# Optimization experiments

Measured on AMD Instinct MI355X. Metric: run time of the kernel, lower is better.

Reference implementation:

```python
import jax, jax.numpy as jnp
import numpy as np

B, T, C, H = 32, 500, 256, 8  # batch, seq, n_embd(=in_c), heads


def setup_inputs() -> dict:
    key = jax.random.key(0)
    ks = jax.random.split(key, 6)
    s = 0.02
    return {
        "x": jax.random.normal(ks[0], (B, T, C), dtype=jnp.float32),
        # nn.Linear(in_c, 3*n_embd): store as [in, out] for x @ W
        "W_attn": jax.random.normal(ks[1], (C, 3 * C), dtype=jnp.float32) * s,
        "b_attn": jnp.zeros((3 * C,), dtype=jnp.float32),
        # nn.Conv1d(heads, 1, 1, bias=False): a per-head mixing weight [H]
        "p_w": jax.random.normal(ks[2], (H,), dtype=jnp.float32) * s,
        # nn.Linear(n_embd, n_embd)
        "W_proj": jax.random.normal(ks[3], (C, C), dtype=jnp.float32) * s,
        "b_proj": jnp.zeros((C,), dtype=jnp.float32),
    }


def reference(x, W_attn, b_attn, p_w, W_proj, b_proj):
    Bx, Tx, Cx = x.shape
    Hh = p_w.shape[0]
    d = Cx // Hh
    qkv = x @ W_attn + b_attn                          # [B,T,3C]
    q, k, v = jnp.split(qkv, 3, axis=-1)
    # [B,T,C] -> [B,H,T,d]
    q = q.reshape(Bx, Tx, Hh, d).transpose(0, 2, 1, 3)
    k = k.reshape(Bx, Tx, Hh, d).transpose(0, 2, 1, 3)
    v = v.reshape(Bx, Tx, Hh, d).transpose(0, 2, 1, 3)
    scale = 1.0 / np.sqrt(d).astype(np.float32)
    att = jnp.einsum('bhtd,bhsd->bhts', q, k) * scale  # [B,H,T,T]
    # bias buffer is all ones for T<=500, so masked_fill is a no-op
    # pred path: 1x1 conv over heads (weighted sum), then sigmoid
    pred_weight = jax.nn.sigmoid(jnp.einsum('bhts,h->bts', att, p_w))  # [B,T,T]
    pred_weight = jnp.where(jnp.isnan(pred_weight), 0.0, pred_weight)
    # value path: softmax @ V
    a = jax.nn.softmax(att, axis=-1)                   # [B,H,T,T]
    ctx = jnp.einsum('bhts,bhsd->bhtd', a, v)          # [B,H,T,d]
    ctx = ctx.transpose(0, 2, 1, 3).reshape(Bx, Tx, Cx)  # [B,T,C]
    value = ctx @ W_proj + b_proj
    return (pred_weight, value)
```

## Files before the change

kernel.cpp:

```cpp
#include <hip/hip_runtime.h>
#include <stddef.h>

typedef unsigned short u16;
typedef unsigned int u32;
typedef __attribute__((ext_vector_type(4))) float f32x4;
typedef __attribute__((ext_vector_type(8))) u16 u16x8;
typedef __attribute__((ext_vector_type(8))) short s16x8;
typedef __attribute__((ext_vector_type(2))) u32 u32x2;
typedef __attribute__((ext_vector_type(4))) u32 u32x4;

#define MFMA16 __builtin_amdgcn_mfma_f32_16x16x32_bf16

__device__ __forceinline__ float bf2f(u16 u) { return __uint_as_float(((u32)u) << 16); }
__device__ __forceinline__ u16 f2bf(float f) {
  u32 u = __float_as_uint(f);
  return (u16)((u + 0x7FFFu + ((u >> 16) & 1u)) >> 16);
}
__device__ __forceinline__ u32 cvt_pk_bf16(float lo, float hi) {
  u32 r; asm("v_cvt_pk_bf16_f32 %0, %1, %2" : "=v"(r) : "v"(lo), "v"(hi)); return r;
}
__device__ __forceinline__ float lo16f(u32 v) { return __uint_as_float(v << 16); }
__device__ __forceinline__ float hi16f(u32 v) { return __uint_as_float(v & 0xffff0000u); }

union frag_u { u32x4 u; s16x8 s; };


__global__ __launch_bounds__(256) void convert_x(
    const float* __restrict__ x, u16* __restrict__ xb)
{
  size_t i = ((size_t)blockIdx.x * 256 + threadIdx.x) * 8;
  f32x4 a = *(const f32x4*)&x[i];
  f32x4 b = *(const f32x4*)&x[i + 4];
  u32x4 o;
  o[0] = cvt_pk_bf16(a[0], a[1]); o[1] = cvt_pk_bf16(a[2], a[3]);
  o[2] = cvt_pk_bf16(b[0], b[1]); o[3] = cvt_pk_bf16(b[2], b[3]);
  *(u32x4*)&xb[i] = o;
}

__global__ __launch_bounds__(256) void gemm_qkv(
    const u16* __restrict__ xbA, const float* __restrict__ W,
    const float* __restrict__ bias, u16* __restrict__ qkbuf, u16* __restrict__ vt)
{
  __shared__ u16 As[128][32];
  __shared__ u16 Bs[64][40];
  const int tid = threadIdx.x;
  const int lane = tid & 63;
  const int w = tid >> 6;
  const int cl = lane & 15, g = lane >> 4;
  const int m0 = blockIdx.x * 128, n0 = blockIdx.y * 64;
  const int wm = w >> 1, wn = w & 1;
  const int bn = tid & 63, bk8 = (tid >> 6) * 8;
  const int ar0 = tid >> 2, ac0 = (tid & 3) * 8;
  const int ar1 = (tid + 256) >> 2, ac1 = ((tid + 256) & 3) * 8;

  f32x4 acc[4][2];
#pragma unroll
  for (int mi = 0; mi < 4; ++mi)
#pragma unroll
    for (int ni = 0; ni < 2; ++ni) acc[mi][ni] = (f32x4){0.f, 0.f, 0.f, 0.f};

  for (int kt = 0; kt < 8; ++kt) {
    const int k0 = kt * 32;
    u16x8 a0 = *(const u16x8*)&xbA[(size_t)(m0 + ar0) * 256 + k0 + ac0];
    u16x8 a1 = *(const u16x8*)&xbA[(size_t)(m0 + ar1) * 256 + k0 + ac1];
    float wv[8];
#pragma unroll
    for (int j = 0; j < 8; ++j)
      wv[j] = W[(size_t)(k0 + bk8 + j) * 768 + n0 + bn];
    __syncthreads();
    *(u16x8*)&As[ar0][ac0] = a0;
    *(u16x8*)&As[ar1][ac1] = a1;
    u32x4 bw;
    bw[0] = cvt_pk_bf16(wv[0], wv[1]); bw[1] = cvt_pk_bf16(wv[2], wv[3]);
    bw[2] = cvt_pk_bf16(wv[4], wv[5]); bw[3] = cvt_pk_bf16(wv[6], wv[7]);
    *(u32x4*)&Bs[bn][bk8] = bw;
    __syncthreads();
    s16x8 af[4], bfr[2];
#pragma unroll
    for (int mi = 0; mi < 4; ++mi) af[mi] = *(const s16x8*)&As[wm * 64 + mi * 16 + cl][g * 8];
#pragma unroll
    for (int ni = 0; ni < 2; ++ni) bfr[ni] = *(const s16x8*)&Bs[wn * 32 + ni * 16 + cl][g * 8];
#pragma unroll
    for (int mi = 0; mi < 4; ++mi)
#pragma unroll
      for (int ni = 0; ni < 2; ++ni)
        acc[mi][ni] = MFMA16(af[mi], bfr[ni], acc[mi][ni], 0, 0, 0);
  }
  float bb[2] = { bias[n0 + wn * 32 + cl], bias[n0 + wn * 32 + 16 + cl] };
  if (n0 < 512) {
#pragma unroll
    for (int mi = 0; mi < 4; ++mi)
#pragma unroll
      for (int ni = 0; ni < 2; ++ni)
#pragma unroll
        for (int r = 0; r < 4; ++r) {
          int m = m0 + wm * 64 + mi * 16 + g * 4 + r;
          qkbuf[(size_t)m * 512 + n0 + wn * 32 + ni * 16 + cl] = f2bf(acc[mi][ni][r] + bb[ni]);
        }
  } else {
#pragma unroll
    for (int mi = 0; mi < 4; ++mi)
#pragma unroll
      for (int ni = 0; ni < 2; ++ni) {
        int cb = n0 - 512 + wn * 32 + ni * 16 + cl;
#pragma unroll
        for (int r = 0; r < 4; ++r) {
          int m = m0 + wm * 64 + mi * 16 + g * 4 + r;
          int b2 = m / 500;
          int t2 = m - b2 * 500;
          vt[(size_t)(b2 * 256 + cb) * 500 + t2] = f2bf(acc[mi][ni][r] + bb[ni]);
        }
      }
  }
}

__global__ __launch_bounds__(256) void gemm_proj(
    const u16* __restrict__ A, const float* __restrict__ W,
    const float* __restrict__ bias, float* __restrict__ out)
{
  __shared__ u16 As[128][32];
  __shared__ u16 Bs[64][40];
  const int tid = threadIdx.x;
  const int lane = tid & 63;
  const int w = tid >> 6;
  const int cl = lane & 15, g = lane >> 4;
  const int m0 = blockIdx.x * 128, n0 = blockIdx.y * 64;
  const int wm = w >> 1, wn = w & 1;
  const int bn = tid & 63, bk8 = (tid >> 6) * 8;
  const int ar0 = tid >> 2, ac0 = (tid & 3) * 8;
  const int ar1 = (tid + 256) >> 2, ac1 = ((tid + 256) & 3) * 8;

  f32x4 acc[4][2];
#pragma unroll
  for (int mi = 0; mi < 4; ++mi)
#pragma unroll
    for (int ni = 0; ni < 2; ++ni) acc[mi][ni] = (f32x4){0.f, 0.f, 0.f, 0.f};

  for (int kt = 0; kt < 8; ++kt) {
    const int k0 = kt * 32;
    u16x8 a0 = *(const u16x8*)&A[(size_t)(m0 + ar0) * 256 + k0 + ac0];
    u16x8 a1 = *(const u16x8*)&A[(size_t)(m0 + ar1) * 256 + k0 + ac1];
    float wv[8];
#pragma unroll
    for (int j = 0; j < 8; ++j)
      wv[j] = W[(size_t)(k0 + bk8 + j) * 256 + n0 + bn];
    __syncthreads();
    *(u16x8*)&As[ar0][ac0] = a0;
    *(u16x8*)&As[ar1][ac1] = a1;
    u32x4 bw;
    bw[0] = cvt_pk_bf16(wv[0], wv[1]); bw[1] = cvt_pk_bf16(wv[2], wv[3]);
    bw[2] = cvt_pk_bf16(wv[4], wv[5]); bw[3] = cvt_pk_bf16(wv[6], wv[7]);
    *(u32x4*)&Bs[bn][bk8] = bw;
    __syncthreads();
    s16x8 af[4], bfr[2];
#pragma unroll
    for (int mi = 0; mi < 4; ++mi) af[mi] = *(const s16x8*)&As[wm * 64 + mi * 16 + cl][g * 8];
#pragma unroll
    for (int ni = 0; ni < 2; ++ni) bfr[ni] = *(const s16x8*)&Bs[wn * 32 + ni * 16 + cl][g * 8];
#pragma unroll
    for (int mi = 0; mi < 4; ++mi)
#pragma unroll
      for (int ni = 0; ni < 2; ++ni)
        acc[mi][ni] = MFMA16(af[mi], bfr[ni], acc[mi][ni], 0, 0, 0);
  }
  float bb[2] = { bias[n0 + wn * 32 + cl], bias[n0 + wn * 32 + 16 + cl] };
#pragma unroll
  for (int mi = 0; mi < 4; ++mi)
#pragma unroll
    for (int ni = 0; ni < 2; ++ni)
#pragma unroll
      for (int r = 0; r < 4; ++r) {
        int m = m0 + wm * 64 + mi * 16 + g * 4 + r;
        out[(size_t)m * 256 + n0 + wn * 32 + ni * 16 + cl] = acc[mi][ni][r] + bb[ni];
      }
}

__global__ __launch_bounds__(512, 3) void attn_mfma2(
    const u16* __restrict__ qk, const u16* __restrict__ vt,
    const float* __restrict__ pw_g, float* __restrict__ pred, u16* __restrict__ ctx)
{
  __shared__ u32 pred_lds[8][64][20];
  const int tid = threadIdx.x;
  const int w = tid >> 6;
  const int lane = tid & 63;
  const int cl = lane & 15;
  const int g = lane >> 4;
  const int lin = blockIdx.x;
  const int b = (lin & 7) * 4 + ((lin >> 3) >> 4);
  const int t0 = ((lin >> 3) & 15) * 32;
  const float scale = 0.17677669529663687f;
  const float pwh = pw_g[w] * scale;

  const u16* qkb = qk + (size_t)b * 500 * 512;
  const u16* vtb = vt + (size_t)b * 256 * 500;

  s16x8 qf[2];
#pragma unroll
  for (int qi = 0; qi < 2; ++qi) {
    int tq = t0 + qi * 16 + cl; if (tq > 499) tq = 499;
    qf[qi] = *(const s16x8*)&qkb[(size_t)tq * 512 + w * 32 + g * 8];
  }
  s16x8 onesf;
#pragma unroll
  for (int j = 0; j < 8; ++j) onesf[j] = (short)0x3F80;

  f32x4 of[2][2], lf[2];
#pragma unroll
  for (int qi = 0; qi < 2; ++qi) {
    lf[qi] = (f32x4){0.f, 0.f, 0.f, 0.f};
    of[qi][0] = (f32x4){0.f, 0.f, 0.f, 0.f};
    of[qi][1] = (f32x4){0.f, 0.f, 0.f, 0.f};
  }

  const int rq = tid >> 4;
  const int rs4 = tid & 15;
  const int rsrc = (rs4 & 3) * 16 + (rq & 15);
  const int ridx = (rq >> 4) * 8 + (rs4 >> 2) * 2;
  const int sA = (g & 1) * 32 + cl;
  const int sB = sA + 16;
  const bool hiHalf = (lane >= 32);

#pragma unroll 1
  for (int st = 0; st < 8; ++st) {
    const int s0 = st * 64;
    f32x4 St[2][4];
    {
      s16x8 kf[4];
#pragma unroll
      for (int si = 0; si < 4; ++si) {
        int sr = s0 + si * 16 + cl; if (sr > 499) sr = 499;
        kf[si] = *(const s16x8*)&qkb[(size_t)sr * 512 + 256 + w * 32 + g * 8];
      }
      const f32x4 zf = (f32x4){0.f, 0.f, 0.f, 0.f};
#pragma unroll
      for (int qi = 0; qi < 2; ++qi)
#pragma unroll
        for (int si = 0; si < 4; ++si)
          St[qi][si] = MFMA16(kf[si], qf[qi], zf, 0, 0, 0);
    }
    s16x8 vf[2][2];
#pragma unroll
    for (int di = 0; di < 2; ++di)
#pragma unroll
      for (int s32 = 0; s32 < 2; ++s32) {
        int sv = s0 + s32 * 32 + g * 8; if (sv > 499) sv = 464;
        vf[di][s32] = *(const s16x8*)&vtb[(size_t)(w * 32 + di * 16 + cl) * 500 + sv];
      }
    u32 P2[2][4][2], PD[2][4][2];
#pragma unroll
    for (int qi = 0; qi < 2; ++qi)
#pragma unroll
      for (int si = 0; si < 4; ++si) {
        float pv[4], pdv[4];
#pragma unroll
        for (int r = 0; r < 4; ++r) {
          int sidx = s0 + si * 16 + g * 4 + r;
          float sraw = St[qi][si][r];
          pdv[r] = sraw * pwh;
          float e = __expf(sraw * scale);
          pv[r] = (sidx < 500) ? e : 0.f;
        }
        P2[qi][si][0] = cvt_pk_bf16(pv[0], pv[1]);
        P2[qi][si][1] = cvt_pk_bf16(pv[2], pv[3]);
        PD[qi][si][0] = cvt_pk_bf16(pdv[0], pdv[1]);
        PD[qi][si][1] = cvt_pk_bf16(pdv[2], pdv[3]);
      }
    {
      u32* wp = &pred_lds[w][lane][0];
      u32x4 v0, v1, v2, v3;
      v0[0] = PD[0][0][0]; v0[1] = PD[0][0][1]; v0[2] = PD[0][1][0]; v0[3] = PD[0][1][1];
      v1[0] = PD[0][2][0]; v1[1] = PD[0][2][1]; v1[2] = PD[0][3][0]; v1[3] = PD[0][3][1];
      v2[0] = PD[1][0][0]; v2[1] = PD[1][0][1]; v2[2] = PD[1][1][0]; v2[3] = PD[1][1][1];
      v3[0] = PD[1][2][0]; v3[1] = PD[1][2][1]; v3[2] = PD[1][3][0]; v3[3] = PD[1][3][1];
      *(u32x4*)(wp + 0) = v0;  *(u32x4*)(wp + 4) = v1;
      *(u32x4*)(wp + 8) = v2;  *(u32x4*)(wp + 12) = v3;
    }
#pragma unroll
    for (int s32 = 0; s32 < 2; ++s32) {
#pragma unroll
      for (int qi = 0; qi < 2; ++qi) {
        u32 Z0 = hiHalf ? P2[qi][2 * s32 + 1][0] : P2[qi][2 * s32][0];
        u32 Z1 = hiHalf ? P2[qi][2 * s32 + 1][1] : P2[qi][2 * s32][1];
        frag_u fu;
        fu.u[0] = (u32)__shfl((int)Z0, sA);
        fu.u[1] = (u32)__shfl((int)Z1, sA);
        fu.u[2] = (u32)__shfl((int)Z0, sB);
        fu.u[3] = (u32)__shfl((int)Z1, sB);
        of[qi][0] = MFMA16(fu.s, vf[0][s32], of[qi][0], 0, 0, 0);
        of[qi][1] = MFMA16(fu.s, vf[1][s32], of[qi][1], 0, 0, 0);
        lf[qi] = MFMA16(fu.s, onesf, lf[qi], 0, 0, 0);
      }
    }
    __syncthreads();
    {
      float a0 = 0.f, a1 = 0.f, a2 = 0.f, a3 = 0.f;
#pragma unroll
      for (int w8 = 0; w8 < 8; ++w8) {
        u32x2 v = *(const u32x2*)&pred_lds[w8][rsrc][ridx];
        a0 += lo16f(v[0]); a1 += hi16f(v[0]);
        a2 += lo16f(v[1]); a3 += hi16f(v[1]);
      }
      int tq = t0 + rq, ss = s0 + rs4 * 4;
      if (tq < 500 && ss < 500) {
        f32x4 o;
        o[0] = 1.f / (1.f + __expf(-a0));
        o[1] = 1.f / (1.f + __expf(-a1));
        o[2] = 1.f / (1.f + __expf(-a2));
        o[3] = 1.f / (1.f + __expf(-a3));
        *(f32x4*)&pred[(size_t)(b * 500 + tq) * 500 + ss] = o;
      }
    }
    __syncthreads();
  }
#pragma unroll
  for (int qi = 0; qi < 2; ++qi)
#pragma unroll
    for (int r = 0; r < 4; ++r) {
      int tq = t0 + qi * 16 + g * 4 + r;
      if (tq < 500) {
        float inv = 1.f / lf[qi][r];
        ctx[(size_t)(b * 500 + tq) * 256 + w * 32 + cl]      = f2bf(of[qi][0][r] * inv);
        ctx[(size_t)(b * 500 + tq) * 256 + w * 32 + 16 + cl] = f2bf(of[qi][1][r] * inv);
      }
    }
}

extern "C" void kernel_launch(void* const* d_in, const int* in_sizes, int n_in,
                              void* d_out, int out_size, void* d_ws, size_t ws_size,
                              hipStream_t stream)
{
  const float* x      = (const float*)d_in[0];
  const float* W_attn = (const float*)d_in[1];
  const float* b_attn = (const float*)d_in[2];
  const float* p_w    = (const float*)d_in[3];
  const float* W_proj = (const float*)d_in[4];
  const float* b_proj = (const float*)d_in[5];

  float* pred   = (float*)d_out;
  float* valout = pred + 8000000;

  u16* xb    = (u16*)d_ws;
  u16* ctx   = xb;
  u16* vt    = (u16*)((char*)d_ws + 8192000);
  u16* qkbuf = (u16*)((char*)d_ws + 16384000);

  hipLaunchKernelGGL(convert_x, dim3(2000), dim3(256), 0, stream, x, xb);
  hipLaunchKernelGGL(gemm_qkv, dim3(125, 12), dim3(256), 0, stream,
                     xb, W_attn, b_attn, qkbuf, vt);
  hipLaunchKernelGGL(attn_mfma2, dim3(512), dim3(512), 0, stream,
                     qkbuf, vt, p_w, pred, ctx);
  hipLaunchKernelGGL(gemm_proj, dim3(125, 4), dim3(256), 0, stream,
                     ctx, W_proj, b_proj, valout);
}
```

Measured before the change: 93.68 us.

## Split fused attention into separate pred GEMM and value-attention kernels

Replaces the single fused attention kernel, which reduced per-head scores across waves through LDS with two block barriers per step, with two kernels. The first computes the head-weighted pred scores as a GEMM over all heads, scaling each per-head MFMA partial by p_w. The second handles softmax@V per head with a shuffle-reduced row sum instead of an MFMA against a ones vector. It also folds the fp32-to-bf16 conversion of x into the QKV GEMM load, dropping the convert kernel. The trade-off is recomputing QK^T in both kernels and one extra launch.

```diff
diff --git a/kernel.cpp b/kernel.cpp
--- a/kernel.cpp
+++ b/kernel.cpp
@@ -6,7 +6,6 @@
 typedef __attribute__((ext_vector_type(4))) float f32x4;
 typedef __attribute__((ext_vector_type(8))) u16 u16x8;
 typedef __attribute__((ext_vector_type(8))) short s16x8;
-typedef __attribute__((ext_vector_type(2))) u32 u32x2;
 typedef __attribute__((ext_vector_type(4))) u32 u32x4;
 
 #define MFMA16 __builtin_amdgcn_mfma_f32_16x16x32_bf16
@@ -19,26 +18,12 @@
 __device__ __forceinline__ u32 cvt_pk_bf16(float lo, float hi) {
   u32 r; asm("v_cvt_pk_bf16_f32 %0, %1, %2" : "=v"(r) : "v"(lo), "v"(hi)); return r;
 }
-__device__ __forceinline__ float lo16f(u32 v) { return __uint_as_float(v << 16); }
-__device__ __forceinline__ float hi16f(u32 v) { return __uint_as_float(v & 0xffff0000u); }
 
 union frag_u { u32x4 u; s16x8 s; };
 
 
-__global__ __launch_bounds__(256) void convert_x(
-    const float* __restrict__ x, u16* __restrict__ xb)
-{
-  size_t i = ((size_t)blockIdx.x * 256 + threadIdx.x) * 8;
-  f32x4 a = *(const f32x4*)&x[i];
-  f32x4 b = *(const f32x4*)&x[i + 4];
-  u32x4 o;
-  o[0] = cvt_pk_bf16(a[0], a[1]); o[1] = cvt_pk_bf16(a[2], a[3]);
-  o[2] = cvt_pk_bf16(b[0], b[1]); o[3] = cvt_pk_bf16(b[2], b[3]);
-  *(u32x4*)&xb[i] = o;
-}
-
 __global__ __launch_bounds__(256) void gemm_qkv(
-    const u16* __restrict__ xbA, const float* __restrict__ W,
+    const float* __restrict__ x, const float* __restrict__ W,
     const float* __restrict__ bias, u16* __restrict__ qkbuf, u16* __restrict__ vt)
 {
   __shared__ u16 As[128][32];
@@ -61,15 +46,22 @@
 
   for (int kt = 0; kt < 8; ++kt) {
     const int k0 = kt * 32;
-    u16x8 a0 = *(const u16x8*)&xbA[(size_t)(m0 + ar0) * 256 + k0 + ac0];
-    u16x8 a1 = *(const u16x8*)&xbA[(size_t)(m0 + ar1) * 256 + k0 + ac1];
+    f32x4 a0l = *(const f32x4*)&x[(size_t)(m0 + ar0) * 256 + k0 + ac0];
+    f32x4 a0h = *(const f32x4*)&x[(size_t)(m0 + ar0) * 256 + k0 + ac0 + 4];
+    f32x4 a1l = *(const f32x4*)&x[(size_t)(m0 + ar1) * 256 + k0 + ac1];
+    f32x4 a1h = *(const f32x4*)&x[(size_t)(m0 + ar1) * 256 + k0 + ac1 + 4];
     float wv[8];
 #pragma unroll
     for (int j = 0; j < 8; ++j)
       wv[j] = W[(size_t)(k0 + bk8 + j) * 768 + n0 + bn];
     __syncthreads();
-    *(u16x8*)&As[ar0][ac0] = a0;
-    *(u16x8*)&As[ar1][ac1] = a1;
+    u32x4 p0, p1;
+    p0[0] = cvt_pk_bf16(a0l[0], a0l[1]); p0[1] = cvt_pk_bf16(a0l[2], a0l[3]);
+    p0[2] = cvt_pk_bf16(a0h[0], a0h[1]); p0[3] = cvt_pk_bf16(a0h[2], a0h[3]);
+    p1[0] = cvt_pk_bf16(a1l[0], a1l[1]); p1[1] = cvt_pk_bf16(a1l[2], a1l[3]);
+    p1[2] = cvt_pk_bf16(a1h[0], a1h[1]); p1[3] = cvt_pk_bf16(a1h[2], a1h[3]);
+    *(u32x4*)&As[ar0][ac0] = p0;
+    *(u32x4*)&As[ar1][ac1] = p1;
     u32x4 bw;
     bw[0] = cvt_pk_bf16(wv[0], wv[1]); bw[1] = cvt_pk_bf16(wv[2], wv[3]);
     bw[2] = cvt_pk_bf16(wv[4], wv[5]); bw[3] = cvt_pk_bf16(wv[6], wv[7]);
@@ -111,6 +103,177 @@
           vt[(size_t)(b2 * 256 + cb) * 500 + t2] = f2bf(acc[mi][ni][r] + bb[ni]);
         }
       }
+  }
+}
+
+__global__ __launch_bounds__(256) void pred_gemm(
+    const u16* __restrict__ qk, const float* __restrict__ pw_g,
+    float* __restrict__ pred)
+{
+  const int tid = threadIdx.x;
+  const int lane = tid & 63;
+  const int w = tid >> 6;
+  const int cl = lane & 15, g = lane >> 4;
+  const int lin = blockIdx.x;
+  const int xcd = lin & 7, idx = lin >> 3;
+  const int b = xcd * 4 + (idx >> 4);
+  const int tile = idx & 15;
+  const int tm = tile >> 2, tn = tile & 3;
+  const int r0 = tm * 128 + (w >> 1) * 64;
+  const int c0 = tn * 128 + (w & 1) * 64;
+  const float scale = 0.17677669529663687f;
+
+  const u16* qkb = qk + (size_t)b * 500 * 512;
+  float fw[8];
+#pragma unroll
+  for (int h = 0; h < 8; ++h) fw[h] = pw_g[h] * scale;
+
+  f32x4 acc[4][4];
+#pragma unroll
+  for (int mi = 0; mi < 4; ++mi)
+#pragma unroll
+    for (int ni = 0; ni < 4; ++ni) acc[mi][ni] = (f32x4){0.f, 0.f, 0.f, 0.f};
+
+#pragma unroll 2
+  for (int kt = 0; kt < 8; ++kt) {
+    const int k0 = kt * 32;
+    s16x8 af[4], bf[4];
+#pragma unroll
+    for (int mi = 0; mi < 4; ++mi) {
+      int t = r0 + mi * 16 + cl; if (t > 499) t = 499;
+      af[mi] = *(const s16x8*)&qkb[(size_t)t * 512 + k0 + g * 8];
+    }
+#pragma unroll
+    for (int ni = 0; ni < 4; ++ni) {
+      int s = c0 + ni * 16 + cl; if (s > 499) s = 499;
+      bf[ni] = *(const s16x8*)&qkb[(size_t)s * 512 + 256 + k0 + g * 8];
+    }
+    const f32x4 zf = (f32x4){0.f, 0.f, 0.f, 0.f};
+    const float f = fw[kt];
+#pragma unroll
+    for (int mi = 0; mi < 4; ++mi)
+#pragma unroll
+      for (int ni = 0; ni < 4; ++ni) {
+        f32x4 part = MFMA16(af[mi], bf[ni], zf, 0, 0, 0);
+#pragma unroll
+        for (int r = 0; r < 4; ++r) acc[mi][ni][r] = fmaf(f, part[r], acc[mi][ni][r]);
+      }
+  }
+#pragma unroll
+  for (int mi = 0; mi < 4; ++mi)
+#pragma unroll
+    for (int ni = 0; ni < 4; ++ni) {
+      const int s = c0 + ni * 16 + cl;
+#pragma unroll
+      for (int r = 0; r < 4; ++r) {
+        const int t = r0 + mi * 16 + g * 4 + r;
+        if (t < 500 && s < 500) {
+          pred[(size_t)(b * 500 + t) * 500 + s] =
+              1.f / (1.f + __expf(-acc[mi][ni][r]));
+        }
+      }
+    }
+}
+
+__global__ __launch_bounds__(256) void attn_value(
+    const u16* __restrict__ qk, const u16* __restrict__ vt, u16* __restrict__ ctx)
+{
+  const int tid = threadIdx.x;
+  const int w = tid >> 6;
+  const int lane = tid & 63;
+  const int cl = lane & 15, g = lane >> 4;
+  const int lin = blockIdx.x;
+  const int xcd = lin & 7, idx = lin >> 3;
+  const int b = xcd * 4 + (idx >> 5);
+  const int rem = idx & 31;
+  const int h = rem >> 2, qg = rem & 3;
+  const int t0 = qg * 128 + w * 32;
+  const float scale = 0.17677669529663687f;
+
+  const u16* qkb = qk + (size_t)b * 500 * 512;
+  const u16* vtb = vt + (size_t)b * 256 * 500;
+
+  s16x8 qf[2];
+#pragma unroll
+  for (int qi = 0; qi < 2; ++qi) {
+    int tq = t0 + qi * 16 + cl; if (tq > 499) tq = 499;
+    qf[qi] = *(const s16x8*)&qkb[(size_t)tq * 512 + h * 32 + g * 8];
+  }
+  f32x4 of[2][2];
+  float lsum[2] = {0.f, 0.f};
+#pragma unroll
+  for (int qi = 0; qi < 2; ++qi) {
+    of[qi][0] = (f32x4){0.f, 0.f, 0.f, 0.f};
+    of[qi][1] = (f32x4){0.f, 0.f, 0.f, 0.f};
+  }
+  const int sA = (g & 1) * 32 + cl;
+  const int sB = sA + 16;
+  const bool hiHalf = (lane >= 32);
+
+#pragma unroll 1
+  for (int st = 0; st < 8; ++st) {
+    const int s0 = st * 64;
+    s16x8 kf[4];
+#pragma unroll
+    for (int si = 0; si < 4; ++si) {
+      int sr = s0 + si * 16 + cl; if (sr > 499) sr = 499;
+      kf[si] = *(const s16x8*)&qkb[(size_t)sr * 512 + 256 + h * 32 + g * 8];
+    }
+    s16x8 vf[2][2];
+#pragma unroll
+    for (int di = 0; di < 2; ++di)
+#pragma unroll
+      for (int s32 = 0; s32 < 2; ++s32)
+        vf[di][s32] = *(const s16x8*)&vtb[(size_t)(h * 32 + di * 16 + cl) * 500 +
+                                          s0 + s32 * 32 + g * 8];
+    const f32x4 zf = (f32x4){0.f, 0.f, 0.f, 0.f};
+    u32 P2[2][4][2];
+#pragma unroll
+    for (int qi = 0; qi < 2; ++qi) {
+#pragma unroll
+      for (int si = 0; si < 4; ++si) {
+        f32x4 St = MFMA16(kf[si], qf[qi], zf, 0, 0, 0);
+        float pv[4];
+#pragma unroll
+        for (int r = 0; r < 4; ++r) {
+          int sidx = s0 + si * 16 + g * 4 + r;
+          float e = __expf(St[r] * scale);
+          pv[r] = (sidx < 500) ? e : 0.f;
+          lsum[qi] += pv[r];
+        }
+        P2[qi][si][0] = cvt_pk_bf16(pv[0], pv[1]);
+        P2[qi][si][1] = cvt_pk_bf16(pv[2], pv[3]);
+      }
+    }
+#pragma unroll
+    for (int s32 = 0; s32 < 2; ++s32) {
+#pragma unroll
+      for (int qi = 0; qi < 2; ++qi) {
+        u32 Z0 = hiHalf ? P2[qi][2 * s32 + 1][0] : P2[qi][2 * s32][0];
+        u32 Z1 = hiHalf ? P2[qi][2 * s32 + 1][1] : P2[qi][2 * s32][1];
+        frag_u fu;
+        fu.u[0] = (u32)__shfl((int)Z0, sA);
+        fu.u[1] = (u32)__shfl((int)Z1, sA);
+        fu.u[2] = (u32)__shfl((int)Z0, sB);
+        fu.u[3] = (u32)__shfl((int)Z1, sB);
+        of[qi][0] = MFMA16(fu.s, vf[0][s32], of[qi][0], 0, 0, 0);
+        of[qi][1] = MFMA16(fu.s, vf[1][s32], of[qi][1], 0, 0, 0);
+      }
+    }
+  }
+#pragma unroll
+  for (int qi = 0; qi < 2; ++qi) {
+    float l2 = lsum[qi] + __shfl_xor(lsum[qi], 16);
+    l2 += __shfl_xor(l2, 32);
+#pragma unroll
+    for (int r = 0; r < 4; ++r) {
+      const int tq = t0 + qi * 16 + g * 4 + r;
+      if (tq < 500) {
+        const float inv = 1.f / __shfl(l2, g * 4 + r);
+        ctx[(size_t)(b * 500 + tq) * 256 + h * 32 + cl]      = f2bf(of[qi][0][r] * inv);
+        ctx[(size_t)(b * 500 + tq) * 256 + h * 32 + 16 + cl] = f2bf(of[qi][1][r] * inv);
+      }
+    }
   }
 }
 
@@ -175,156 +338,6 @@
       }
 }
 
-__global__ __launch_bounds__(512, 3) void attn_mfma2(
-    const u16* __restrict__ qk, const u16* __restrict__ vt,
-    const float* __restrict__ pw_g, float* __restrict__ pred, u16* __restrict__ ctx)
-{
-  __shared__ u32 pred_lds[8][64][20];
-  const int tid = threadIdx.x;
-  const int w = tid >> 6;
-  const int lane = tid & 63;
-  const int cl = lane & 15;
-  const int g = lane >> 4;
-  const int lin = blockIdx.x;
-  const int b = (lin & 7) * 4 + ((lin >> 3) >> 4);
-  const int t0 = ((lin >> 3) & 15) * 32;
-  const float scale = 0.17677669529663687f;
-  const float pwh = pw_g[w] * scale;
-
-  const u16* qkb = qk + (size_t)b * 500 * 512;
-  const u16* vtb = vt + (size_t)b * 256 * 500;
-
-  s16x8 qf[2];
-#pragma unroll
-  for (int qi = 0; qi < 2; ++qi) {
-    int tq = t0 + qi * 16 + cl; if (tq > 499) tq = 499;
-    qf[qi] = *(const s16x8*)&qkb[(size_t)tq * 512 + w * 32 + g * 8];
-  }
-  s16x8 onesf;
-#pragma unroll
-  for (int j = 0; j < 8; ++j) onesf[j] = (short)0x3F80;
-
-  f32x4 of[2][2], lf[2];
-#pragma unroll
-  for (int qi = 0; qi < 2; ++qi) {
-    lf[qi] = (f32x4){0.f, 0.f, 0.f, 0.f};
-    of[qi][0] = (f32x4){0.f, 0.f, 0.f, 0.f};
-    of[qi][1] = (f32x4){0.f, 0.f, 0.f, 0.f};
-  }
-
-  const int rq = tid >> 4;
-  const int rs4 = tid & 15;
-  const int rsrc = (rs4 & 3) * 16 + (rq & 15);
-  const int ridx = (rq >> 4) * 8 + (rs4 >> 2) * 2;
-  const int sA = (g & 1) * 32 + cl;
-  const int sB = sA + 16;
-  const bool hiHalf = (lane >= 32);
-
-#pragma unroll 1
-  for (int st = 0; st < 8; ++st) {
-    const int s0 = st * 64;
-    f32x4 St[2][4];
-    {
-      s16x8 kf[4];
-#pragma unroll
-      for (int si = 0; si < 4; ++si) {
-        int sr = s0 + si * 16 + cl; if (sr > 499) sr = 499;
-        kf[si] = *(const s16x8*)&qkb[(size_t)sr * 512 + 256 + w * 32 + g * 8];
-      }
-      const f32x4 zf = (f32x4){0.f, 0.f, 0.f, 0.f};
-#pragma unroll
-      for (int qi = 0; qi < 2; ++qi)
-#pragma unroll
-        for (int si = 0; si < 4; ++si)
-          St[qi][si] = MFMA16(kf[si], qf[qi], zf, 0, 0, 0);
-    }
-    s16x8 vf[2][2];
-#pragma unroll
-    for (int di = 0; di < 2; ++di)
-#pragma unroll
-      for (int s32 = 0; s32 < 2; ++s32) {
-        int sv = s0 + s32 * 32 + g * 8; if (sv > 499) sv = 464;
-        vf[di][s32] = *(const s16x8*)&vtb[(size_t)(w * 32 + di * 16 + cl) * 500 + sv];
-      }
-    u32 P2[2][4][2], PD[2][4][2];
-#pragma unroll
-    for (int qi = 0; qi < 2; ++qi)
-#pragma unroll
-      for (int si = 0; si < 4; ++si) {
-        float pv[4], pdv[4];
-#pragma unroll
-        for (int r = 0; r < 4; ++r) {
-          int sidx = s0 + si * 16 + g * 4 + r;
-          float sraw = St[qi][si][r];
-          pdv[r] = sraw * pwh;
-          float e = __expf(sraw * scale);
-          pv[r] = (sidx < 500) ? e : 0.f;
-        }
-        P2[qi][si][0] = cvt_pk_bf16(pv[0], pv[1]);
-        P2[qi][si][1] = cvt_pk_bf16(pv[2], pv[3]);
-        PD[qi][si][0] = cvt_pk_bf16(pdv[0], pdv[1]);
-        PD[qi][si][1] = cvt_pk_bf16(pdv[2], pdv[3]);
-      }
-    {
-      u32* wp = &pred_lds[w][lane][0];
-      u32x4 v0, v1, v2, v3;
-      v0[0] = PD[0][0][0]; v0[1] = PD[0][0][1]; v0[2] = PD[0][1][0]; v0[3] = PD[0][1][1];
-      v1[0] = PD[0][2][0]; v1[1] = PD[0][2][1]; v1[2] = PD[0][3][0]; v1[3] = PD[0][3][1];
-      v2[0] = PD[1][0][0]; v2[1] = PD[1][0][1]; v2[2] = PD[1][1][0]; v2[3] = PD[1][1][1];
-      v3[0] = PD[1][2][0]; v3[1] = PD[1][2][1]; v3[2] = PD[1][3][0]; v3[3] = PD[1][3][1];
-      *(u32x4*)(wp + 0) = v0;  *(u32x4*)(wp + 4) = v1;
-      *(u32x4*)(wp + 8) = v2;  *(u32x4*)(wp + 12) = v3;
-    }
-#pragma unroll
-    for (int s32 = 0; s32 < 2; ++s32) {
-#pragma unroll
-      for (int qi = 0; qi < 2; ++qi) {
-        u32 Z0 = hiHalf ? P2[qi][2 * s32 + 1][0] : P2[qi][2 * s32][0];
-        u32 Z1 = hiHalf ? P2[qi][2 * s32 + 1][1] : P2[qi][2 * s32][1];
-        frag_u fu;
-        fu.u[0] = (u32)__shfl((int)Z0, sA);
-        fu.u[1] = (u32)__shfl((int)Z1, sA);
-        fu.u[2] = (u32)__shfl((int)Z0, sB);
-        fu.u[3] = (u32)__shfl((int)Z1, sB);
-        of[qi][0] = MFMA16(fu.s, vf[0][s32], of[qi][0], 0, 0, 0);
-        of[qi][1] = MFMA16(fu.s, vf[1][s32], of[qi][1], 0, 0, 0);
-        lf[qi] = MFMA16(fu.s, onesf, lf[qi], 0, 0, 0);
-      }
-    }
-    __syncthreads();
-    {
-      float a0 = 0.f, a1 = 0.f, a2 = 0.f, a3 = 0.f;
-#pragma unroll
-      for (int w8 = 0; w8 < 8; ++w8) {
-        u32x2 v = *(const u32x2*)&pred_lds[w8][rsrc][ridx];
-        a0 += lo16f(v[0]); a1 += hi16f(v[0]);
-        a2 += lo16f(v[1]); a3 += hi16f(v[1]);
-      }
-      int tq = t0 + rq, ss = s0 + rs4 * 4;
-      if (tq < 500 && ss < 500) {
-        f32x4 o;
-        o[0] = 1.f / (1.f + __expf(-a0));
-        o[1] = 1.f / (1.f + __expf(-a1));
-        o[2] = 1.f / (1.f + __expf(-a2));
-        o[3] = 1.f / (1.f + __expf(-a3));
-        *(f32x4*)&pred[(size_t)(b * 500 + tq) * 500 + ss] = o;
-      }
-    }
-    __syncthreads();
-  }
-#pragma unroll
-  for (int qi = 0; qi < 2; ++qi)
-#pragma unroll
-    for (int r = 0; r < 4; ++r) {
-      int tq = t0 + qi * 16 + g * 4 + r;
-      if (tq < 500) {
-        float inv = 1.f / lf[qi][r];
-        ctx[(size_t)(b * 500 + tq) * 256 + w * 32 + cl]      = f2bf(of[qi][0][r] * inv);
-        ctx[(size_t)(b * 500 + tq) * 256 + w * 32 + 16 + cl] = f2bf(of[qi][1][r] * inv);
-      }
-    }
-}
-
 extern "C" void kernel_launch(void* const* d_in, const int* in_sizes, int n_in,
                               void* d_out, int out_size, void* d_ws, size_t ws_size,
                               hipStream_t stream)
@@ -339,16 +352,16 @@
   float* pred   = (float*)d_out;
   float* valout = pred + 8000000;
 
-  u16* xb    = (u16*)d_ws;
-  u16* ctx   = xb;
-  u16* vt    = (u16*)((char*)d_ws + 8192000);
-  u16* qkbuf = (u16*)((char*)d_ws + 16384000);
-
-  hipLaunchKernelGGL(convert_x, dim3(2000), dim3(256), 0, stream, x, xb);
+  u16* qkbuf = (u16*)d_ws;
+  u16* vt    = (u16*)((char*)d_ws + 16384000);
+  u16* ctx   = (u16*)((char*)d_ws + 24576000);
+
   hipLaunchKernelGGL(gemm_qkv, dim3(125, 12), dim3(256), 0, stream,
-                     xb, W_attn, b_attn, qkbuf, vt);
-  hipLaunchKernelGGL(attn_mfma2, dim3(512), dim3(512), 0, stream,
-                     qkbuf, vt, p_w, pred, ctx);
+                     x, W_attn, b_attn, qkbuf, vt);
+  hipLaunchKernelGGL(pred_gemm, dim3(512), dim3(256), 0, stream,
+                     qkbuf, p_w, pred);
+  hipLaunchKernelGGL(attn_value, dim3(1024), dim3(256), 0, stream,
+                     qkbuf, vt, ctx);
   hipLaunchKernelGGL(gemm_proj, dim3(125, 4), dim3(256), 0, stream,
                      ctx, W_proj, b_proj, valout);
 }
```

Measured after the change: 104.3 us. +11.3%, slower.
